# Kernel optimization log

Hardware: AMD Instinct MI355X
Metric: run time of the kernel (lower is better)

The kernel has to match this reference:

```python
import jax, jax.numpy as jnp
import numpy as np

VEC, H, B, S = 768, 256, 64, 512


def setup_inputs() -> dict:
    key = jax.random.key(0)
    ks = jax.random.split(key, 8)
    sc = 0.02
    return {
        "output_1": jax.random.normal(ks[0], (B, S, VEC), dtype=jnp.float32),
        "output_2": jax.random.normal(ks[1], (B, S, VEC), dtype=jnp.float32),
        "mlp_w": jax.random.normal(ks[2], (H, VEC), dtype=jnp.float32) * sc,
        "mlp_b": jnp.zeros((H,), dtype=jnp.float32),
        "fd_w": jax.random.normal(ks[3], (H, 2 * H), dtype=jnp.float32) * sc,
        "fd_b": jnp.zeros((H,), dtype=jnp.float32),
        "ff_w": jax.random.normal(ks[4], (1, H), dtype=jnp.float32) * sc,
        "ff_b": jnp.zeros((1,), dtype=jnp.float32),
    }


def reference(output_1, output_2, mlp_w, mlp_b, fd_w, fd_b, ff_w, ff_b):
    # eval-mode forward of Bert_coss
    o1 = jax.nn.relu(output_1 @ mlp_w.T + mlp_b)        # [B,S,H]
    o2 = jax.nn.relu(output_2 @ mlp_w.T + mlp_b)        # [B,S,H]
    o1_doc = jnp.mean(o1, axis=1)                        # [B,H]
    o2_doc = jnp.mean(o2, axis=1)                        # [B,H]
    h = jax.nn.relu(jnp.concatenate([o1_doc, o2_doc], axis=1) @ fd_w.T + fd_b)
    out = jax.nn.sigmoid(jnp.squeeze(h @ ff_w.T + ff_b))  # [B]
    # append doc vectors as an extra token
    o1e = jnp.concatenate([o1, o1_doc[:, None, :]], axis=1)  # [B,S+1,H]
    o2e = jnp.concatenate([o2, o2_doc[:, None, :]], axis=1)  # [B,S+1,H]
    # graph_match: scores + softmax over dim=1; only last column is used downstream
    a = jnp.einsum('bsh,bth->bst', o1e, o2e)             # [B,S+1,S+1]
    a_x = jax.nn.softmax(a, axis=1)
    att = a_x[:, :, -1].T                                # [S+1,B]
    att = jnp.concatenate([att[:-1], out[None, :]], axis=0)  # [S+1,B]
    return att
```

## Files before the change

### kernel.cpp

```cpp
#include <hip/hip_runtime.h>
#include <hip/hip_bf16.h>
#include <math.h>

#define B_ 64
#define S_ 512
#define VEC_ 768
#define H_ 256
#define M_ (B_*S_)

typedef float floatx4 __attribute__((ext_vector_type(4)));
typedef __bf16 bf16x8 __attribute__((ext_vector_type(8)));
typedef __bf16 bf16x4 __attribute__((ext_vector_type(4)));

#define STRIDE 40

__global__ __launch_bounds__(256) void prep_kernel(
    const float* __restrict__ mlp_w, __bf16* __restrict__ wbf, float* __restrict__ sums)
{
  const int bid = blockIdx.x;
  if (bid < 192) {
    const int i = bid * 256 + threadIdx.x;
    const float4 v = ((const float4*)mlp_w)[i];
    bf16x4 b = { (__bf16)v.x, (__bf16)v.y, (__bf16)v.z, (__bf16)v.w };
    *(bf16x4*)&wbf[(size_t)i * 4] = b;
  } else {
    const int i = (bid - 192) * 256 + threadIdx.x;
    ((float4*)sums)[i] = make_float4(0.f, 0.f, 0.f, 0.f);
  }
}

__global__ __launch_bounds__(256) void gemm_doc_kernel(
    const float* __restrict__ out1, const float* __restrict__ out2,
    const __bf16* __restrict__ wbf, const float* __restrict__ mlp_b,
    __bf16* __restrict__ o1, float* __restrict__ sum1, float* __restrict__ sum2)
{
  __shared__ __align__(16) __bf16 As[128 * STRIDE];
  __shared__ __align__(16) __bf16 Bs[128 * STRIDE];

  const int tensor = blockIdx.z;
  const float* __restrict__ A = tensor ? out2 : out1;
  float* __restrict__ dsum = tensor ? sum2 : sum1;

  const int n0 = blockIdx.x * 128;
  const int m0 = blockIdx.y * 128;
  const int bidx = m0 >> 9;

  const int t = threadIdx.x;
  const int lane = t & 63;
  const int wave = t >> 6;
  const int q = lane >> 4;
  const int c = lane & 15;
  const int wm = (wave >> 1) * 64;
  const int wn = (wave & 1) * 64;

  floatx4 acc[4][4];
  for (int i = 0; i < 4; i++)
    for (int j = 0; j < 4; j++)
      acc[i][j] = (floatx4){0.f, 0.f, 0.f, 0.f};

  float4 aR[4];
  bf16x8 bR[2];

  {
    const float* Ab = &A[(size_t)m0 * VEC_];
    const __bf16* Wb = &wbf[(size_t)n0 * VEC_];
#pragma unroll
    for (int i = 0; i < 4; i++) {
      const int ch = t + i * 256;
      aR[i] = *(const float4*)&Ab[(size_t)(ch >> 3) * VEC_ + (ch & 7) * 4];
    }
#pragma unroll
    for (int i = 0; i < 2; i++) {
      const int ch = t + i * 256;
      bR[i] = *(const bf16x8*)&Wb[(size_t)(ch >> 2) * VEC_ + (ch & 3) * 8];
    }
  }

#pragma unroll 1
  for (int k0 = 0; k0 < VEC_; k0 += 32) {
#pragma unroll
    for (int i = 0; i < 4; i++) {
      const int ch = t + i * 256;
      bf16x4 v = { (__bf16)aR[i].x, (__bf16)aR[i].y, (__bf16)aR[i].z, (__bf16)aR[i].w };
      *(bf16x4*)&As[(ch >> 3) * STRIDE + (ch & 7) * 4] = v;
    }
#pragma unroll
    for (int i = 0; i < 2; i++) {
      const int ch = t + i * 256;
      *(bf16x8*)&Bs[(ch >> 2) * STRIDE + (ch & 3) * 8] = bR[i];
    }
    if (k0 + 32 < VEC_) {
      const float* Ab = &A[(size_t)m0 * VEC_ + k0 + 32];
      const __bf16* Wb = &wbf[(size_t)n0 * VEC_ + k0 + 32];
#pragma unroll
      for (int i = 0; i < 4; i++) {
        const int ch = t + i * 256;
        aR[i] = *(const float4*)&Ab[(size_t)(ch >> 3) * VEC_ + (ch & 7) * 4];
      }
#pragma unroll
      for (int i = 0; i < 2; i++) {
        const int ch = t + i * 256;
        bR[i] = *(const bf16x8*)&Wb[(size_t)(ch >> 2) * VEC_ + (ch & 3) * 8];
      }
    }
    __syncthreads();
    bf16x8 af[4], bfr[4];
#pragma unroll
    for (int i = 0; i < 4; i++) af[i]  = *(const bf16x8*)&As[(wm + i * 16 + c) * STRIDE + q * 8];
#pragma unroll
    for (int j = 0; j < 4; j++) bfr[j] = *(const bf16x8*)&Bs[(wn + j * 16 + c) * STRIDE + q * 8];
#pragma unroll
    for (int i = 0; i < 4; i++)
#pragma unroll
      for (int j = 0; j < 4; j++)
        acc[i][j] = __builtin_amdgcn_mfma_f32_16x16x32_bf16(af[i], bfr[j], acc[i][j], 0, 0, 0);
    __syncthreads();
  }

#pragma unroll
  for (int j = 0; j < 4; j++) {
    const int n = n0 + wn + j * 16 + c;
    const float bias = mlp_b[n];
    float colsum = 0.f;
#pragma unroll
    for (int i = 0; i < 4; i++) {
      const int mbase = m0 + wm + i * 16 + q * 4;
#pragma unroll
      for (int r = 0; r < 4; r++) {
        float v = acc[i][j][r] + bias;
        v = fmaxf(v, 0.f);
        colsum += v;
        if (tensor == 0) o1[(size_t)(mbase + r) * H_ + n] = (__bf16)v;
      }
    }
    colsum += __shfl_down(colsum, 32);
    colsum += __shfl_down(colsum, 16);
    if (lane < 16)
      atomicAdd(&dsum[bidx * H_ + n0 + wn + j * 16 + lane], colsum);
  }
}

__global__ __launch_bounds__(256) void logits_kernel(
    const __bf16* __restrict__ o1, const float* __restrict__ sum1,
    const float* __restrict__ sum2, float* __restrict__ lg)
{
  const int b = blockIdx.y;
  const int schunk = blockIdx.x;
  const int t = threadIdx.x, lane = t & 63, wave = t >> 6;
  __shared__ __align__(16) float o2d[256];
  if (t < 256) o2d[t] = sum2[b * H_ + t] * (1.f / 512.f);
  __syncthreads();
  const float4 w = ((const float4*)o2d)[lane];
  const int sbase = schunk * 64;
  for (int s = sbase + wave; s < sbase + 64; s += 4) {
    const bf16x4 x = *(const bf16x4*)&o1[((size_t)b * S_ + s) * H_ + lane * 4];
    float p = (float)x[0] * w.x + (float)x[1] * w.y + (float)x[2] * w.z + (float)x[3] * w.w;
    p += __shfl_down(p, 32); p += __shfl_down(p, 16); p += __shfl_down(p, 8);
    p += __shfl_down(p, 4);  p += __shfl_down(p, 2);  p += __shfl_down(p, 1);
    if (lane == 0) lg[b * 513 + s] = p;
  }
  if (schunk == 0 && wave == 0) {
    const float4 x = ((const float4*)&sum1[b * H_])[lane];
    float p = (x.x * w.x + x.y * w.y + x.z * w.z + x.w * w.w) * (1.f / 512.f);
    p += __shfl_down(p, 32); p += __shfl_down(p, 16); p += __shfl_down(p, 8);
    p += __shfl_down(p, 4);  p += __shfl_down(p, 2);  p += __shfl_down(p, 1);
    if (lane == 0) lg[b * 513 + 512] = p;
  }
}

__global__ __launch_bounds__(256) void softmax_head_kernel(
    const float* __restrict__ lg, const float* __restrict__ sum1, const float* __restrict__ sum2,
    const float* __restrict__ fd_w, const float* __restrict__ fd_b,
    const float* __restrict__ ff_w, const float* __restrict__ ff_b,
    float* __restrict__ out)
{
  const int b = blockIdx.x, t = threadIdx.x, lane = t & 63, wave = t >> 6;
  __shared__ __align__(16) float dc[512];
  __shared__ float sl[513];
  __shared__ float red[4], r1[4], r2[4];

  dc[t]       = sum1[b * H_ + t] * (1.f / 512.f);
  dc[t + 256] = sum2[b * H_ + t] * (1.f / 512.f);
  for (int i = t; i < 513; i += 256) sl[i] = lg[b * 513 + i];
  __syncthreads();
  const float4* wrow = (const float4*)&fd_w[(size_t)t * 512];
  const float4* dc4  = (const float4*)dc;
  float acc = 0.f;
  for (int k = 0; k < 128; k++) {
    const float4 w = wrow[k], d = dc4[k];
    acc += w.x * d.x + w.y * d.y + w.z * d.z + w.w * d.w;
  }
  const float h = fmaxf(acc + fd_b[t], 0.f);
  float part = ff_w[t] * h;
  part += __shfl_down(part, 32); part += __shfl_down(part, 16);
  part += __shfl_down(part, 8);  part += __shfl_down(part, 4);
  part += __shfl_down(part, 2);  part += __shfl_down(part, 1);
  if (lane == 0) red[wave] = part;

  float m = -1e30f;
  for (int i = t; i < 513; i += 256) m = fmaxf(m, sl[i]);
  m = fmaxf(m, __shfl_down(m, 32)); m = fmaxf(m, __shfl_down(m, 16));
  m = fmaxf(m, __shfl_down(m, 8));  m = fmaxf(m, __shfl_down(m, 4));
  m = fmaxf(m, __shfl_down(m, 2));  m = fmaxf(m, __shfl_down(m, 1));
  if (lane == 0) r1[wave] = m;
  __syncthreads();
  m = fmaxf(fmaxf(r1[0], r1[1]), fmaxf(r1[2], r1[3]));
  float psum = 0.f;
  for (int i = t; i < 513; i += 256) { const float e = expf(sl[i] - m); sl[i] = e; psum += e; }
  psum += __shfl_down(psum, 32); psum += __shfl_down(psum, 16); psum += __shfl_down(psum, 8);
  psum += __shfl_down(psum, 4);  psum += __shfl_down(psum, 2);  psum += __shfl_down(psum, 1);
  if (lane == 0) r2[wave] = psum;
  __syncthreads();
  const float inv = 1.f / (r2[0] + r2[1] + r2[2] + r2[3]);
  for (int s = t; s < 512; s += 256) out[s * 64 + b] = sl[s] * inv;
  if (t == 0) {
    const float tot = red[0] + red[1] + red[2] + red[3] + ff_b[0];
    out[(size_t)512 * 64 + b] = 1.f / (1.f + expf(-tot));
  }
}

extern "C" void kernel_launch(void* const* d_in, const int* in_sizes, int n_in,
                              void* d_out, int out_size, void* d_ws, size_t ws_size,
                              hipStream_t stream) {
  const float* out1  = (const float*)d_in[0];
  const float* out2  = (const float*)d_in[1];
  const float* mlp_w = (const float*)d_in[2];
  const float* mlp_b = (const float*)d_in[3];
  const float* fd_w  = (const float*)d_in[4];
  const float* fd_b  = (const float*)d_in[5];
  const float* ff_w  = (const float*)d_in[6];
  const float* ff_b  = (const float*)d_in[7];
  float* out = (float*)d_out;

  __bf16* o1  = (__bf16*)d_ws;
  __bf16* wbf = o1 + (size_t)M_ * H_;
  float*  s1  = (float*)(wbf + (size_t)H_ * VEC_);
  float*  s2  = s1 + B_ * H_;
  float*  lgw = s2 + B_ * H_;

  prep_kernel<<<224, 256, 0, stream>>>(mlp_w, wbf, s1);
  gemm_doc_kernel<<<dim3(2, 256, 2), 256, 0, stream>>>(out1, out2, wbf, mlp_b, o1, s1, s2);
  logits_kernel<<<dim3(8, B_), 256, 0, stream>>>(o1, s1, s2, lgw);
  softmax_head_kernel<<<B_, 256, 0, stream>>>(lgw, s1, s2, fd_w, fd_b, ff_w, ff_b, out);
}
```

Baseline: 284.0 us.

## Double-buffer GEMM with direct global-to-LDS loads and swizzled layout

The GEMM kernel now stages A (fp32) and B (bf16) tiles straight from global memory into a double-buffered, XOR-swizzled LDS region using global_load_lds. The fp32-to-bf16 conversion moves to LDS read time, and the next tile loads while the current one computes. The aim is to stop routing tiles through registers, to overlap loads with MFMA work, and to avoid LDS bank conflicts, at the cost of 48KB of LDS and twice as many LDS bytes for A. It also gives each wave in the logits kernel a single row across a larger grid, and splits the head dot product into two accumulators.

```diff
diff --git a/kernel.cpp b/kernel.cpp
--- a/kernel.cpp
+++ b/kernel.cpp
@@ -11,8 +11,6 @@
 typedef float floatx4 __attribute__((ext_vector_type(4)));
 typedef __bf16 bf16x8 __attribute__((ext_vector_type(8)));
 typedef __bf16 bf16x4 __attribute__((ext_vector_type(4)));
-
-#define STRIDE 40
 
 __global__ __launch_bounds__(256) void prep_kernel(
     const float* __restrict__ mlp_w, __bf16* __restrict__ wbf, float* __restrict__ sums)
@@ -29,13 +27,70 @@
   }
 }
 
-__global__ __launch_bounds__(256) void gemm_doc_kernel(
+#define ABUF_ 16384
+#define BUFB_ 24576
+#define LDSB_ 49152
+
+__device__ __forceinline__ void gl_lds16(char* l, const void* g) {
+  __builtin_amdgcn_global_load_lds(
+      (const __attribute__((address_space(1))) unsigned int*)g,
+      (__attribute__((address_space(3))) unsigned int*)l, 16, 0, 0);
+}
+
+#define STAGE(bufbase, kk)                                                    \
+  {                                                                           \
+    _Pragma("unroll")                                                         \
+    for (int i_ = 0; i_ < 4; i_++) {                \
+      const int ch = t + i_ * 256;                                            \
+      const int row = ch >> 3;                                                \
+      const int cc = (ch & 7) ^ (row & 7);     \
+      gl_lds16(smem + (bufbase) + ch * 16,                                    \
+               Abase + (size_t)row * VEC_ + (kk) + cc * 4);                   \
+    }                                                                         \
+    _Pragma("unroll")                                                         \
+    for (int i_ = 0; i_ < 2; i_++) {                 \
+      const int ch = t + i_ * 256;                                            \
+      const int row = ch >> 2;                                                \
+      const int cc = ((ch & 3) ^ row ^ (row >> 2)) & 3;                       \
+      gl_lds16(smem + (bufbase) + ABUF_ + ch * 16,                            \
+               Bbase + (size_t)row * VEC_ + (kk) + cc * 8);                   \
+    }                                                                         \
+  }
+
+#define COMPUTE(bufbase)                                                      \
+  {                                                                           \
+    const char* Ab = smem + (bufbase);                                        \
+    const char* Bb = smem + (bufbase) + ABUF_;                                \
+    bf16x8 af[4]; bf16x8 bfr[4];                                              \
+    _Pragma("unroll")                                                         \
+    for (int i = 0; i < 4; i++) {                                             \
+      const int base = (wm + i * 16 + c) * 128;                               \
+      const floatx4 a0 = *(const floatx4*)(Ab + base + aslot0);               \
+      const floatx4 a1 = *(const floatx4*)(Ab + base + (aslot0 ^ 16));        \
+      bf16x8 v;                                                               \
+      v[0] = (__bf16)a0[0]; v[1] = (__bf16)a0[1];                             \
+      v[2] = (__bf16)a0[2]; v[3] = (__bf16)a0[3];                             \
+      v[4] = (__bf16)a1[0]; v[5] = (__bf16)a1[1];                             \
+      v[6] = (__bf16)a1[2]; v[7] = (__bf16)a1[3];                             \
+      af[i] = v;                                                              \
+    }                                                                         \
+    _Pragma("unroll")                                                         \
+    for (int j = 0; j < 4; j++)                                               \
+      bfr[j] = *(const bf16x8*)(Bb + (wn + j * 16 + c) * 64 + bslot);         \
+    _Pragma("unroll")                                                         \
+    for (int i = 0; i < 4; i++)                                               \
+      _Pragma("unroll")                                                       \
+      for (int j = 0; j < 4; j++)                                             \
+        acc[i][j] = __builtin_amdgcn_mfma_f32_16x16x32_bf16(af[i], bfr[j],    \
+                                                            acc[i][j], 0, 0, 0); \
+  }
+
+__global__ __launch_bounds__(256, 3) void gemm_doc_kernel(
     const float* __restrict__ out1, const float* __restrict__ out2,
     const __bf16* __restrict__ wbf, const float* __restrict__ mlp_b,
     __bf16* __restrict__ o1, float* __restrict__ sum1, float* __restrict__ sum2)
 {
-  __shared__ __align__(16) __bf16 As[128 * STRIDE];
-  __shared__ __align__(16) __bf16 Bs[128 * STRIDE];
+  __shared__ __align__(16) char smem[LDSB_];
 
   const int tensor = blockIdx.z;
   const float* __restrict__ A = tensor ? out2 : out1;
@@ -53,69 +108,33 @@
   const int wm = (wave >> 1) * 64;
   const int wn = (wave & 1) * 64;
 
+  const int aslot0 = (((2 * q) ^ (c & 7)) << 4);
+  const int bslot  = (((q ^ c ^ (c >> 2)) & 3) << 4);
+
+  const float* Abase = &A[(size_t)m0 * VEC_];
+  const __bf16* Bbase = &wbf[(size_t)n0 * VEC_];
+
   floatx4 acc[4][4];
+#pragma unroll
   for (int i = 0; i < 4; i++)
+#pragma unroll
     for (int j = 0; j < 4; j++)
       acc[i][j] = (floatx4){0.f, 0.f, 0.f, 0.f};
 
-  float4 aR[4];
-  bf16x8 bR[2];
-
-  {
-    const float* Ab = &A[(size_t)m0 * VEC_];
-    const __bf16* Wb = &wbf[(size_t)n0 * VEC_];
-#pragma unroll
-    for (int i = 0; i < 4; i++) {
-      const int ch = t + i * 256;
-      aR[i] = *(const float4*)&Ab[(size_t)(ch >> 3) * VEC_ + (ch & 7) * 4];
-    }
-#pragma unroll
-    for (int i = 0; i < 2; i++) {
-      const int ch = t + i * 256;
-      bR[i] = *(const bf16x8*)&Wb[(size_t)(ch >> 2) * VEC_ + (ch & 3) * 8];
-    }
-  }
-
+  STAGE(0, 0);
+  __syncthreads();
+
+  int bufb = 0;
+  int kk = 32;
 #pragma unroll 1
-  for (int k0 = 0; k0 < VEC_; k0 += 32) {
-#pragma unroll
-    for (int i = 0; i < 4; i++) {
-      const int ch = t + i * 256;
-      bf16x4 v = { (__bf16)aR[i].x, (__bf16)aR[i].y, (__bf16)aR[i].z, (__bf16)aR[i].w };
-      *(bf16x4*)&As[(ch >> 3) * STRIDE + (ch & 7) * 4] = v;
-    }
-#pragma unroll
-    for (int i = 0; i < 2; i++) {
-      const int ch = t + i * 256;
-      *(bf16x8*)&Bs[(ch >> 2) * STRIDE + (ch & 3) * 8] = bR[i];
-    }
-    if (k0 + 32 < VEC_) {
-      const float* Ab = &A[(size_t)m0 * VEC_ + k0 + 32];
-      const __bf16* Wb = &wbf[(size_t)n0 * VEC_ + k0 + 32];
-#pragma unroll
-      for (int i = 0; i < 4; i++) {
-        const int ch = t + i * 256;
-        aR[i] = *(const float4*)&Ab[(size_t)(ch >> 3) * VEC_ + (ch & 7) * 4];
-      }
-#pragma unroll
-      for (int i = 0; i < 2; i++) {
-        const int ch = t + i * 256;
-        bR[i] = *(const bf16x8*)&Wb[(size_t)(ch >> 2) * VEC_ + (ch & 3) * 8];
-      }
-    }
+  for (int kt = 0; kt < 23; ++kt) {
+    STAGE(bufb ^ BUFB_, kk);
+    COMPUTE(bufb);
+    kk += 32;
     __syncthreads();
-    bf16x8 af[4], bfr[4];
-#pragma unroll
-    for (int i = 0; i < 4; i++) af[i]  = *(const bf16x8*)&As[(wm + i * 16 + c) * STRIDE + q * 8];
-#pragma unroll
-    for (int j = 0; j < 4; j++) bfr[j] = *(const bf16x8*)&Bs[(wn + j * 16 + c) * STRIDE + q * 8];
-#pragma unroll
-    for (int i = 0; i < 4; i++)
-#pragma unroll
-      for (int j = 0; j < 4; j++)
-        acc[i][j] = __builtin_amdgcn_mfma_f32_16x16x32_bf16(af[i], bfr[j], acc[i][j], 0, 0, 0);
-    __syncthreads();
-  }
+    bufb ^= BUFB_;
+  }
+  COMPUTE(bufb);
 
 #pragma unroll
   for (int j = 0; j < 4; j++) {
@@ -145,27 +164,23 @@
     const float* __restrict__ sum2, float* __restrict__ lg)
 {
   const int b = blockIdx.y;
-  const int schunk = blockIdx.x;
   const int t = threadIdx.x, lane = t & 63, wave = t >> 6;
-  __shared__ __align__(16) float o2d[256];
-  if (t < 256) o2d[t] = sum2[b * H_ + t] * (1.f / 512.f);
-  __syncthreads();
-  const float4 w = ((const float4*)o2d)[lane];
-  const int sbase = schunk * 64;
-  for (int s = sbase + wave; s < sbase + 64; s += 4) {
-    const bf16x4 x = *(const bf16x4*)&o1[((size_t)b * S_ + s) * H_ + lane * 4];
-    float p = (float)x[0] * w.x + (float)x[1] * w.y + (float)x[2] * w.z + (float)x[3] * w.w;
-    p += __shfl_down(p, 32); p += __shfl_down(p, 16); p += __shfl_down(p, 8);
-    p += __shfl_down(p, 4);  p += __shfl_down(p, 2);  p += __shfl_down(p, 1);
-    if (lane == 0) lg[b * 513 + s] = p;
-  }
-  if (schunk == 0 && wave == 0) {
+  const int s = blockIdx.x * 4 + wave;
+  if (s > 512) return;
+  const float sc = 1.f / 512.f;
+  const float4 w4 = ((const float4*)&sum2[b * H_])[lane];
+  float p;
+  if (s < 512) {
+    const bf16x4 x = ((const bf16x4*)&o1[((size_t)b * S_ + s) * H_])[lane];
+    p = ((float)x[0] * w4.x + (float)x[1] * w4.y +
+         (float)x[2] * w4.z + (float)x[3] * w4.w) * sc;
+  } else {
     const float4 x = ((const float4*)&sum1[b * H_])[lane];
-    float p = (x.x * w.x + x.y * w.y + x.z * w.z + x.w * w.w) * (1.f / 512.f);
-    p += __shfl_down(p, 32); p += __shfl_down(p, 16); p += __shfl_down(p, 8);
-    p += __shfl_down(p, 4);  p += __shfl_down(p, 2);  p += __shfl_down(p, 1);
-    if (lane == 0) lg[b * 513 + 512] = p;
-  }
+    p = (x.x * w4.x + x.y * w4.y + x.z * w4.z + x.w * w4.w) * sc * sc;
+  }
+  p += __shfl_down(p, 32); p += __shfl_down(p, 16); p += __shfl_down(p, 8);
+  p += __shfl_down(p, 4);  p += __shfl_down(p, 2);  p += __shfl_down(p, 1);
+  if (lane == 0) lg[b * 513 + s] = p;
 }
 
 __global__ __launch_bounds__(256) void softmax_head_kernel(
@@ -185,12 +200,15 @@
   __syncthreads();
   const float4* wrow = (const float4*)&fd_w[(size_t)t * 512];
   const float4* dc4  = (const float4*)dc;
-  float acc = 0.f;
-  for (int k = 0; k < 128; k++) {
-    const float4 w = wrow[k], d = dc4[k];
-    acc += w.x * d.x + w.y * d.y + w.z * d.z + w.w * d.w;
-  }
-  const float h = fmaxf(acc + fd_b[t], 0.f);
+  float a0 = 0.f, a1 = 0.f;
+#pragma unroll 8
+  for (int k = 0; k < 128; k += 2) {
+    const float4 w0 = wrow[k],     d0 = dc4[k];
+    const float4 w1 = wrow[k + 1], d1 = dc4[k + 1];
+    a0 += w0.x * d0.x + w0.y * d0.y + w0.z * d0.z + w0.w * d0.w;
+    a1 += w1.x * d1.x + w1.y * d1.y + w1.z * d1.z + w1.w * d1.w;
+  }
+  const float h = fmaxf(a0 + a1 + fd_b[t], 0.f);
   float part = ff_w[t] * h;
   part += __shfl_down(part, 32); part += __shfl_down(part, 16);
   part += __shfl_down(part, 8);  part += __shfl_down(part, 4);
@@ -240,6 +258,6 @@
 
   prep_kernel<<<224, 256, 0, stream>>>(mlp_w, wbf, s1);
   gemm_doc_kernel<<<dim3(2, 256, 2), 256, 0, stream>>>(out1, out2, wbf, mlp_b, o1, s1, s2);
-  logits_kernel<<<dim3(8, B_), 256, 0, stream>>>(o1, s1, s2, lgw);
+  logits_kernel<<<dim3(129, B_), 256, 0, stream>>>(o1, s1, s2, lgw);
   softmax_head_kernel<<<B_, 256, 0, stream>>>(lgw, s1, s2, fd_w, fd_b, ff_w, ff_b, out);
 }
```

Result: slower. 293.9 us (+3.5%).
